# Optimization experiments

Hardware: AMD Instinct MI355X
Metric: run time of the kernel (lower is better)

## Reference

```python
import jax, jax.numpy as jnp
import numpy as np

B, D, M, R, C = 1024, 32, 8, 4096, 32
TOPK_P = 0.1  # hard-coded in torch forward
EPS = 1e-9


def setup_inputs() -> dict:
    key = jax.random.key(0)
    k0, k1, k2, k3, k4 = jax.random.split(key, 5)
    x = jax.random.normal(k0, (B, D), dtype=jnp.float32)
    centers = jax.random.normal(k1, (D, M), dtype=jnp.float32)
    # widths kept away from 0 so gaussian MFs don't all underflow
    widths = jax.random.uniform(k2, (D, M), dtype=jnp.float32, minval=0.5, maxval=1.5)
    consequents = jax.random.uniform(k3, (R, D + 1, C), dtype=jnp.float32)
    rules = jax.random.randint(k4, (R, D), 0, M, dtype=jnp.int32)
    return {"x": x, "centers": centers, "widths": widths,
            "consequents": consequents, "rules": rules}


def reference(x, centers, widths, consequents, rules):
    Bn, Dn = x.shape
    Rn = rules.shape[0]
    # Gaussian membership functions: (B, D, M)
    mfs = jnp.exp(-((x[:, :, None] - centers[None]) ** 2) / (2.0 * widths[None] ** 2))
    # Gather per-rule MF values: (B, D, R)  (torch.gather along mf axis)
    rule_mfs = mfs[:, jnp.arange(Dn)[:, None], rules.T]
    # Firing strengths via product over input dims: (B, R)
    firing = jnp.prod(rule_mfs, axis=1)
    # top-K gate + scatter mask
    K = max(1, int(TOPK_P * Rn))
    _, idx = jax.lax.top_k(firing, K)
    mask = jnp.zeros_like(firing).at[jnp.arange(Bn)[:, None], idx].set(1.0)
    firing = firing * mask
    norm_fs = firing / (firing.sum(axis=1, keepdims=True) + EPS)
    # zeroG=False branch. Torch does einsum('bi,rjc->brc', x_ext, consequents)
    # which sums i and j independently: rule_mfs[b,r,c] = sum_i(x_ext[b,i]) * sum_j(cons[r,j,c]).
    # Then einsum('br,brc->bc') => out = sum(x_ext,1) * (norm_fs @ sum(cons,1)).
    x_ext_sum = x.sum(axis=1) + 1.0          # sum over x_ext = [x, 1], shape (B,)
    cons_sum = consequents.sum(axis=1)       # (R, C)
    rule_outputs = x_ext_sum[:, None] * (norm_fs @ cons_sum)  # (B, C)
    return rule_outputs, norm_fs, mask
```

## Files before the change

### kernel.cpp

```cpp
#include <hip/hip_runtime.h>

#define Bn 1024
#define Dn 32
#define Mn 8
#define Rn 4096
#define Cn 32
#define Kn 409
#define NTH 512
#define RPT 8
#define NBIN 1024
#define CCAP 256

typedef unsigned int u32;
typedef unsigned short u16;
typedef short bf16x8 __attribute__((ext_vector_type(8)));
typedef float f32x4 __attribute__((ext_vector_type(4)));

__device__ __forceinline__ int binof(float kf) {
    int b = (int)floorf(kf * (float)(NBIN / 120.0) + (float)NBIN);
    return b < 0 ? 0 : (b > NBIN - 1 ? NBIN - 1 : b);
}

__device__ __forceinline__ u16 f2bf(float v) {
    u32 b = __float_as_uint(v);
    b += 0x7fffu + ((b >> 16) & 1u);
    return (u16)(b >> 16);
}

__device__ __forceinline__ double rule_sum_f64(const uint4 q, const double* e) {
    double s = 0.0;
    const u32 wv[4] = {q.x, q.y, q.z, q.w};
#pragma unroll
    for (int p = 0; p < 16; ++p) {
        const u32 byte = (wv[p >> 2] >> (8 * (p & 3))) & 63u;
        s += e[(2 * p) * 8 + (byte & 7u)];
        s += e[(2 * p + 1) * 8 + (byte >> 3)];
    }
    return s;
}

__global__ __launch_bounds__(256) void prep_kernel(
    const float* __restrict__ x, const float* __restrict__ centers,
    const float* __restrict__ widths, const float* __restrict__ cons,
    const int* __restrict__ rules,
    float* __restrict__ cons_out, uint4* __restrict__ packed,
    uint4* __restrict__ S4, uint4* __restrict__ Ehi4, uint4* __restrict__ Elo4)
{
    const int blk = blockIdx.x;
    const int t = threadIdx.x;
    if (blk < 512) {
        const int idx = blk * 256 + t;
        const int r = idx >> 5, c = idx & 31;
        const float* p = cons + (size_t)r * (Dn + 1) * Cn + c;
        float s = 0.0f;
#pragma unroll
        for (int k = 0; k < Dn + 1; ++k) s += p[(size_t)k * Cn];
        cons_out[idx] = s;
    } else if (blk < 528) {
        const int r = (blk - 512) * 256 + t;
        const int* rp = rules + r * Dn;
        u32 w[4];
#pragma unroll
        for (int wi = 0; wi < 4; ++wi) {
            u32 v = 0;
#pragma unroll
            for (int j = 0; j < 4; ++j) {
                const int p = wi * 4 + j;
                v |= (((u32)rp[2 * p] & 7u) | (((u32)rp[2 * p + 1] & 7u) << 3)) << (8 * j);
            }
            w[wi] = v;
        }
        packed[r] = make_uint4(w[0], w[1], w[2], w[3]);
    } else if (blk < 1040) {
        const int r = (blk - 528) * 8 + (t >> 5);
        const int d = t & 31;
        const int v = rules[r * Dn + d];
        uint4 o;
        o.x = (v == 0 ? 0x3F80u : 0u) | (v == 1 ? (0x3F80u << 16) : 0u);
        o.y = (v == 2 ? 0x3F80u : 0u) | (v == 3 ? (0x3F80u << 16) : 0u);
        o.z = (v == 4 ? 0x3F80u : 0u) | (v == 5 ? (0x3F80u << 16) : 0u);
        o.w = (v == 6 ? 0x3F80u : 0u) | (v == 7 ? (0x3F80u << 16) : 0u);
        S4[r * 32 + d] = o;
    } else {
        const int row = (blk - 1040) * 8 + (t >> 5);
        const int d = t & 31;
        const float xv = x[row * Dn + d];
        u16 h[8], l[8];
#pragma unroll
        for (int m = 0; m < 8; ++m) {
            const float c = centers[d * 8 + m];
            const float w = widths[d * 8 + m];
            const float dx = xv - c;
            const float e = -(dx * dx) / (2.f * w * w);
            const u16 hb = f2bf(e);
            h[m] = hb;
            l[m] = f2bf(e - __uint_as_float((u32)hb << 16));
        }
        Ehi4[row * 32 + d] = make_uint4((u32)h[0] | ((u32)h[1] << 16), (u32)h[2] | ((u32)h[3] << 16),
                                        (u32)h[4] | ((u32)h[5] << 16), (u32)h[6] | ((u32)h[7] << 16));
        Elo4[row * 32 + d] = make_uint4((u32)l[0] | ((u32)l[1] << 16), (u32)l[2] | ((u32)l[3] << 16),
                                        (u32)l[4] | ((u32)l[5] << 16), (u32)l[6] | ((u32)l[7] << 16));
    }
}

__global__ __launch_bounds__(256) void key_gemm_kernel(
    const u16* __restrict__ Ehi, const u16* __restrict__ Elo,
    const u16* __restrict__ S, float* __restrict__ keys)
{
    __shared__ u16 sAh[2][128 * 32];
    __shared__ u16 sAl[2][128 * 32];
    __shared__ u16 sB[2][128 * 32];
    const int t = threadIdx.x;
    const int lane = t & 63;
    const int w = t >> 6;
    const int wr = w >> 1, wc = w & 1;
    const int m0 = blockIdx.y * 128;
    const int n0 = blockIdx.x * 128;

    f32x4 acc[4][4];
#pragma unroll
    for (int i = 0; i < 4; ++i)
#pragma unroll
        for (int j = 0; j < 4; ++j) acc[i][j] = (f32x4){0.f, 0.f, 0.f, 0.f};

    const int row1 = t >> 2;
    const int row2 = (t + 256) >> 2;
    const int koff = (t & 3) * 8;

#define GLDS(src, dst) __builtin_amdgcn_global_load_lds( \
        (const __attribute__((address_space(1))) void*)(src), \
        (__attribute__((address_space(3))) void*)(dst), 16, 0, 0)
#define STAGE(buf, k0) do { \
        GLDS(Ehi + (size_t)(m0 + row1) * 256 + (k0) + koff, sAh[buf] + t * 8); \
        GLDS(Ehi + (size_t)(m0 + row2) * 256 + (k0) + koff, sAh[buf] + (t + 256) * 8); \
        GLDS(Elo + (size_t)(m0 + row1) * 256 + (k0) + koff, sAl[buf] + t * 8); \
        GLDS(Elo + (size_t)(m0 + row2) * 256 + (k0) + koff, sAl[buf] + (t + 256) * 8); \
        GLDS(S + (size_t)(n0 + row1) * 256 + (k0) + koff, sB[buf] + t * 8); \
        GLDS(S + (size_t)(n0 + row2) * 256 + (k0) + koff, sB[buf] + (t + 256) * 8); \
    } while (0)

    STAGE(0, 0);
    __syncthreads();
    int cur = 0;
    for (int k0 = 0; k0 < 256; k0 += 32) {
        if (k0 + 32 < 256) STAGE(cur ^ 1, k0 + 32);
        bf16x8 ah[4], al[4], b[4];
#pragma unroll
        for (int mi = 0; mi < 4; ++mi) {
            ah[mi] = *(const bf16x8*)(sAh[cur] + ((wr * 64 + mi * 16 + (lane & 15)) * 32 + (lane >> 4) * 8));
            al[mi] = *(const bf16x8*)(sAl[cur] + ((wr * 64 + mi * 16 + (lane & 15)) * 32 + (lane >> 4) * 8));
        }
#pragma unroll
        for (int ni = 0; ni < 4; ++ni)
            b[ni] = *(const bf16x8*)(sB[cur] + ((wc * 64 + ni * 16 + (lane & 15)) * 32 + (lane >> 4) * 8));
#pragma unroll
        for (int mi = 0; mi < 4; ++mi)
#pragma unroll
            for (int ni = 0; ni < 4; ++ni) {
                acc[mi][ni] = __builtin_amdgcn_mfma_f32_16x16x32_bf16(ah[mi], b[ni], acc[mi][ni], 0, 0, 0);
                acc[mi][ni] = __builtin_amdgcn_mfma_f32_16x16x32_bf16(al[mi], b[ni], acc[mi][ni], 0, 0, 0);
            }
        __syncthreads();
        cur ^= 1;
    }
#undef STAGE
#undef GLDS

    const int cr = (lane >> 4) * 4;
    const int cc = lane & 15;
#pragma unroll
    for (int mi = 0; mi < 4; ++mi)
#pragma unroll
        for (int ni = 0; ni < 4; ++ni)
#pragma unroll
            for (int reg = 0; reg < 4; ++reg)
                keys[(size_t)(m0 + wr * 64 + mi * 16 + cr + reg) * Rn + (n0 + wc * 64 + ni * 16 + cc)] =
                    acc[mi][ni][reg];
}

__global__ __launch_bounds__(NTH, 8) void select_kernel(
    const float* __restrict__ x,
    const float* __restrict__ centers,
    const float* __restrict__ widths,
    const float* __restrict__ keys,
    const uint4* __restrict__ rpack,
    const float* __restrict__ cons_sum,
    float* __restrict__ out_rule,
    float* __restrict__ out_norm,
    float* __restrict__ out_mask)
{
    __shared__ float  s_x[Dn];
    __shared__ double s_e[256];
    __shared__ u32    s_hist[NBIN];
    __shared__ int    s_wtot[8];
    __shared__ float  s_wsum[8];
    __shared__ int    s_wpre[8];
    __shared__ int    s_cidx[CCAP];
    __shared__ double s_cval[CCAP];
    __shared__ int    s_cflag[CCAP];
    __shared__ int    s_selidx[Kn + 8];
    __shared__ float  s_selv[Kn + 8];
    __shared__ float  s_red[NTH];
    __shared__ int    s_bb, s_ccnt;

    const int t = threadIdx.x;
    const int lane = t & 63;
    const int w = t >> 6;
    const int b = blockIdx.x;

    if (t < Dn) s_x[t] = x[b * Dn + t];
    if (t == 0) s_ccnt = 0;
    s_hist[t] = 0u;
    s_hist[t + NTH] = 0u;
    float kf[RPT];
#pragma unroll
    for (int i = 0; i < RPT; ++i) kf[i] = keys[(size_t)b * Rn + i * NTH + t];
    __syncthreads();

    if (t < 256) {
        const int d = t >> 3;
        const double dx = (double)s_x[d] - (double)centers[t];
        const double ww = (double)widths[t];
        s_e[t] = -(dx * dx) / (2.0 * (ww * ww));
    }
#pragma unroll
    for (int i = 0; i < RPT; ++i) atomicAdd(&s_hist[binof(kf[i])], 1u);
    __syncthreads();

    const int h0 = (int)s_hist[2 * t];
    const int h1 = (int)s_hist[2 * t + 1];
    const int loc = h0 + h1;
    int S = loc;
#pragma unroll
    for (int off = 1; off < 64; off <<= 1) {
        const int vv = __shfl(S, lane + off < 64 ? lane + off : lane);
        if (lane + off < 64) S += vv;
    }
    if (lane == 0) s_wtot[w] = S;
    __syncthreads();
    int wsuf = 0;
#pragma unroll
    for (int ww = 0; ww < 8; ++ww) wsuf += (ww > w) ? s_wtot[ww] : 0;
    {
        const int excl = (S - loc) + wsuf;
        const int vtot = excl + loc;
        if (excl < Kn && vtot >= Kn) {
            int c = excl;
            if (c < Kn && c + h1 >= Kn) s_bb = 2 * t + 1;
            c += h1;
            if (c < Kn && c + h0 >= Kn) s_bb = 2 * t;
        }
    }
    __syncthreads();
    const int bb = s_bb;
    const int hi = (bb + 1 > NBIN - 1) ? NBIN - 1 : bb + 1;
    const int lo = (bb - 1 < 0) ? 0 : bb - 1;

    int la = 0;
    if (2 * t > hi) la += h0;
    if (2 * t + 1 > hi) la += h1;
#pragma unroll
    for (int off = 32; off >= 1; off >>= 1) la += __shfl_xor(la, off);
    if (lane == 0) s_wtot[w] = la;
    __syncthreads();
    int Acnt = 0;
#pragma unroll
    for (int ww = 0; ww < 8; ++ww) Acnt += s_wtot[ww];
    const int want_in = Kn - Acnt;

    int mypos[RPT];
#pragma unroll
    for (int i = 0; i < RPT; ++i) {
        mypos[i] = -1;
        const int bn = binof(kf[i]);
        if (bn >= lo && bn <= hi) {
            const int pos = atomicAdd(&s_ccnt, 1);
            if (pos < CCAP) { mypos[i] = pos; s_cidx[pos] = i * NTH + t; }
        }
    }
    __syncthreads();
    const int cnt = s_ccnt < CCAP ? s_ccnt : CCAP;
    if (t < cnt) s_cval[t] = rule_sum_f64(rpack[s_cidx[t]], s_e);
    __syncthreads();
    if (t < cnt) {
        const double mv = s_cval[t];
        const int mi = s_cidx[t];
        int rank = 0;
        for (int j = 0; j < cnt; ++j) {
            const double ov = s_cval[j];
            const int oi = s_cidx[j];
            rank += ((ov > mv) || (ov == mv && oi < mi)) ? 1 : 0;
        }
        s_cflag[t] = (rank < want_in) ? 1 : 0;
    }
    __syncthreads();

    u32 selbits = 0u;
    int cnt_sel = 0;
    float lsum = 0.f;
#pragma unroll
    for (int i = 0; i < RPT; ++i) {
        bool sel = (binof(kf[i]) > hi);
        if (mypos[i] >= 0) sel = (s_cflag[mypos[i]] != 0);
        float f = 0.f;
        if (sel) { f = expf(kf[i]); selbits |= (1u << i); ++cnt_sel; lsum += f; }
        kf[i] = f;
    }
#pragma unroll
    for (int off = 32; off >= 1; off >>= 1) lsum += __shfl_xor(lsum, off);
    if (lane == 0) s_wsum[w] = lsum;
    int p = cnt_sel;
#pragma unroll
    for (int off = 1; off < 64; off <<= 1) {
        const int u = __shfl(p, lane >= off ? lane - off : lane);
        if (lane >= off) p += u;
    }
    if (lane == 63) s_wpre[w] = p;
    __syncthreads();
    float denom = 1e-9f;
#pragma unroll
    for (int ww = 0; ww < 8; ++ww) denom += s_wsum[ww];
    int base = 0;
#pragma unroll
    for (int ww = 0; ww < 8; ++ww) base += (ww < w) ? s_wpre[ww] : 0;
    int pos = base + (p - cnt_sel);

    float* onorm = out_norm + (size_t)b * Rn;
    float* omask = out_mask + (size_t)b * Rn;
#pragma unroll
    for (int i = 0; i < RPT; ++i) {
        const int r = i * NTH + t;
        const bool sel = (selbits >> i) & 1u;
        float nv = 0.f;
        if (sel) {
            nv = kf[i] / denom;
            s_selidx[pos] = r;
            s_selv[pos] = nv;
            ++pos;
        }
        onorm[r] = nv;
        omask[r] = sel ? 1.f : 0.f;
    }
    __syncthreads();

    const int g = t >> 5;
    const int c = t & 31;
    float acc = 0.f;
    for (int i = g; i < Kn; i += 16) {
        acc += s_selv[i] * cons_sum[s_selidx[i] * Cn + c];
    }
    s_red[t] = acc;
    __syncthreads();
    if (t < Cn) {
        float ss = 0.f;
#pragma unroll
        for (int gg = 0; gg < 16; ++gg) ss += s_red[gg * 32 + t];
        float xs = 1.f;
#pragma unroll
        for (int d = 0; d < Dn; ++d) xs += s_x[d];
        out_rule[(size_t)b * Cn + t] = xs * ss;
    }
}

extern "C" void kernel_launch(void* const* d_in, const int* in_sizes, int n_in,
                              void* d_out, int out_size, void* d_ws, size_t ws_size,
                              hipStream_t stream) {
    (void)in_sizes; (void)n_in; (void)out_size; (void)ws_size;
    const float* x = (const float*)d_in[0];
    const float* centers = (const float*)d_in[1];
    const float* widths = (const float*)d_in[2];
    const float* consequents = (const float*)d_in[3];
    const int* rules = (const int*)d_in[4];

    float* out_rule = (float*)d_out;
    float* out_norm = out_rule + (size_t)Bn * Cn;
    float* out_mask = out_norm + (size_t)Bn * Rn;

    char* wsb = (char*)d_ws;
    float* cons_sum = (float*)wsb;
    uint4* rpack = (uint4*)(wsb + (512 << 10));
    u16*   Smat  = (u16*)(wsb + (576 << 10));
    u16*   Ehi   = (u16*)(wsb + (2624 << 10));
    u16*   Elo   = (u16*)(wsb + (3136 << 10));
    float* keys  = (float*)(wsb + (3648 << 10));

    prep_kernel<<<1168, 256, 0, stream>>>(x, centers, widths, consequents, rules,
                                          cons_sum, rpack, (uint4*)Smat, (uint4*)Ehi, (uint4*)Elo);
    dim3 gg(Rn / 128, Bn / 128);
    key_gemm_kernel<<<gg, 256, 0, stream>>>(Ehi, Elo, Smat, keys);
    select_kernel<<<Bn, NTH, 0, stream>>>(x, centers, widths, keys, rpack, cons_sum,
                                          out_rule, out_norm, out_mask);
}
```

Measured before the change: 47.96 us.

## Vectorize select kernel key loads and stores, replace candidate flags with bitmask

The select kernel now loads keys and stores norm/mask outputs as float2 pairs instead of scalar strided accesses. The histogram is turned into a suffix-count array in place, which removes a reduction pass and a barrier when computing the count above the threshold bin. Per-element candidate position tracking is replaced by a shared selection bitmask set with atomicOr. Launch bounds drop from 8 to 4 blocks per SM, and rule indices now interleave pairs per thread, which changes the order of selected rules in the accumulation.

After: 57.73 us. +20.4%, slower.

```diff
diff --git a/kernel.cpp b/kernel.cpp
--- a/kernel.cpp
+++ b/kernel.cpp
@@ -7,7 +7,7 @@
 #define Cn 32
 #define Kn 409
 #define NTH 512
-#define RPT 8
+#define RP2 4
 #define NBIN 1024
 #define CCAP 256
 
@@ -178,7 +178,7 @@
                     acc[mi][ni][reg];
 }
 
-__global__ __launch_bounds__(NTH, 8) void select_kernel(
+__global__ __launch_bounds__(NTH, 4) void select_kernel(
     const float* __restrict__ x,
     const float* __restrict__ centers,
     const float* __restrict__ widths,
@@ -191,13 +191,13 @@
 {
     __shared__ float  s_x[Dn];
     __shared__ double s_e[256];
-    __shared__ u32    s_hist[NBIN];
+    __shared__ u32    s_hist[NBIN + 2];
+    __shared__ u32    s_selmask[Rn / 32];
     __shared__ int    s_wtot[8];
     __shared__ float  s_wsum[8];
     __shared__ int    s_wpre[8];
     __shared__ int    s_cidx[CCAP];
     __shared__ double s_cval[CCAP];
-    __shared__ int    s_cflag[CCAP];
     __shared__ int    s_selidx[Kn + 8];
     __shared__ float  s_selv[Kn + 8];
     __shared__ float  s_red[NTH];
@@ -209,12 +209,14 @@
     const int b = blockIdx.x;
 
     if (t < Dn) s_x[t] = x[b * Dn + t];
-    if (t == 0) s_ccnt = 0;
+    if (t == 0) { s_ccnt = 0; s_hist[NBIN] = 0u; s_hist[NBIN + 1] = 0u; }
     s_hist[t] = 0u;
     s_hist[t + NTH] = 0u;
-    float kf[RPT];
-#pragma unroll
-    for (int i = 0; i < RPT; ++i) kf[i] = keys[(size_t)b * Rn + i * NTH + t];
+    if (t < Rn / 32) s_selmask[t] = 0u;
+    const float2* kptr = (const float2*)(keys + (size_t)b * Rn);
+    float2 kp[RP2];
+#pragma unroll
+    for (int i = 0; i < RP2; ++i) kp[i] = kptr[i * NTH + t];
     __syncthreads();
 
     if (t < 256) {
@@ -224,7 +226,10 @@
         s_e[t] = -(dx * dx) / (2.0 * (ww * ww));
     }
 #pragma unroll
-    for (int i = 0; i < RPT; ++i) atomicAdd(&s_hist[binof(kf[i])], 1u);
+    for (int i = 0; i < RP2; ++i) {
+        atomicAdd(&s_hist[binof(kp[i].x)], 1u);
+        atomicAdd(&s_hist[binof(kp[i].y)], 1u);
+    }
     __syncthreads();
 
     const int h0 = (int)s_hist[2 * t];
@@ -241,41 +246,29 @@
     int wsuf = 0;
 #pragma unroll
     for (int ww = 0; ww < 8; ++ww) wsuf += (ww > w) ? s_wtot[ww] : 0;
-    {
-        const int excl = (S - loc) + wsuf;
-        const int vtot = excl + loc;
-        if (excl < Kn && vtot >= Kn) {
-            int c = excl;
-            if (c < Kn && c + h1 >= Kn) s_bb = 2 * t + 1;
-            c += h1;
-            if (c < Kn && c + h0 >= Kn) s_bb = 2 * t;
-        }
+    const int full = S + wsuf;
+    s_hist[2 * t] = (u32)full;
+    s_hist[2 * t + 1] = (u32)(full - h0);
+    if (full - loc < Kn && full >= Kn) {
+        s_bb = (full - h0 >= Kn) ? (2 * t + 1) : (2 * t);
     }
     __syncthreads();
     const int bb = s_bb;
     const int hi = (bb + 1 > NBIN - 1) ? NBIN - 1 : bb + 1;
     const int lo = (bb - 1 < 0) ? 0 : bb - 1;
-
-    int la = 0;
-    if (2 * t > hi) la += h0;
-    if (2 * t + 1 > hi) la += h1;
-#pragma unroll
-    for (int off = 32; off >= 1; off >>= 1) la += __shfl_xor(la, off);
-    if (lane == 0) s_wtot[w] = la;
-    __syncthreads();
-    int Acnt = 0;
-#pragma unroll
-    for (int ww = 0; ww < 8; ++ww) Acnt += s_wtot[ww];
+    const int Acnt = (int)s_hist[hi + 1];
     const int want_in = Kn - Acnt;
 
-    int mypos[RPT];
-#pragma unroll
-    for (int i = 0; i < RPT; ++i) {
-        mypos[i] = -1;
-        const int bn = binof(kf[i]);
-        if (bn >= lo && bn <= hi) {
-            const int pos = atomicAdd(&s_ccnt, 1);
-            if (pos < CCAP) { mypos[i] = pos; s_cidx[pos] = i * NTH + t; }
+#pragma unroll
+    for (int i = 0; i < RP2; ++i) {
+#pragma unroll
+        for (int j = 0; j < 2; ++j) {
+            const float kf = j ? kp[i].y : kp[i].x;
+            const int bn = binof(kf);
+            if (bn >= lo && bn <= hi) {
+                const int pos = atomicAdd(&s_ccnt, 1);
+                if (pos < CCAP) s_cidx[pos] = i * 1024 + 2 * t + j;
+            }
         }
     }
     __syncthreads();
@@ -291,7 +284,7 @@
             const int oi = s_cidx[j];
             rank += ((ov > mv) || (ov == mv && oi < mi)) ? 1 : 0;
         }
-        s_cflag[t] = (rank < want_in) ? 1 : 0;
+        if (rank < want_in) atomicOr(&s_selmask[mi >> 5], 1u << (mi & 31));
     }
     __syncthreads();
 
@@ -299,12 +292,18 @@
     int cnt_sel = 0;
     float lsum = 0.f;
 #pragma unroll
-    for (int i = 0; i < RPT; ++i) {
-        bool sel = (binof(kf[i]) > hi);
-        if (mypos[i] >= 0) sel = (s_cflag[mypos[i]] != 0);
-        float f = 0.f;
-        if (sel) { f = expf(kf[i]); selbits |= (1u << i); ++cnt_sel; lsum += f; }
-        kf[i] = f;
+    for (int i = 0; i < RP2; ++i) {
+#pragma unroll
+        for (int j = 0; j < 2; ++j) {
+            const float kf = j ? kp[i].y : kp[i].x;
+            const int bn = binof(kf);
+            const int r = i * 1024 + 2 * t + j;
+            bool sel = (bn > hi);
+            if (!sel && bn >= lo) sel = (s_selmask[r >> 5] >> (r & 31)) & 1u;
+            float f = 0.f;
+            if (sel) { f = expf(kf); selbits |= (1u << (2 * i + j)); ++cnt_sel; lsum += f; }
+            if (j) kp[i].y = f; else kp[i].x = f;
+        }
     }
 #pragma unroll
     for (int off = 32; off >= 1; off >>= 1) lsum += __shfl_xor(lsum, off);
@@ -325,21 +324,27 @@
     for (int ww = 0; ww < 8; ++ww) base += (ww < w) ? s_wpre[ww] : 0;
     int pos = base + (p - cnt_sel);
 
-    float* onorm = out_norm + (size_t)b * Rn;
-    float* omask = out_mask + (size_t)b * Rn;
-#pragma unroll
-    for (int i = 0; i < RPT; ++i) {
-        const int r = i * NTH + t;
-        const bool sel = (selbits >> i) & 1u;
-        float nv = 0.f;
-        if (sel) {
-            nv = kf[i] / denom;
-            s_selidx[pos] = r;
-            s_selv[pos] = nv;
-            ++pos;
-        }
-        onorm[r] = nv;
-        omask[r] = sel ? 1.f : 0.f;
+    float2* onorm2 = (float2*)(out_norm + (size_t)b * Rn);
+    float2* omask2 = (float2*)(out_mask + (size_t)b * Rn);
+#pragma unroll
+    for (int i = 0; i < RP2; ++i) {
+        float2 nv2, mk2;
+#pragma unroll
+        for (int j = 0; j < 2; ++j) {
+            const bool sel = (selbits >> (2 * i + j)) & 1u;
+            float nv = 0.f;
+            if (sel) {
+                const float f = j ? kp[i].y : kp[i].x;
+                nv = f / denom;
+                s_selidx[pos] = i * 1024 + 2 * t + j;
+                s_selv[pos] = nv;
+                ++pos;
+            }
+            if (j) { nv2.y = nv; mk2.y = sel ? 1.f : 0.f; }
+            else   { nv2.x = nv; mk2.x = sel ? 1.f : 0.f; }
+        }
+        onorm2[i * NTH + t] = nv2;
+        omask2[i * NTH + t] = mk2;
     }
     __syncthreads();
 
```
